# Optimization experiments

Measured on AMD Instinct MI355X. Metric: run time of the kernel, lower is better.

## Reference

```python
import jax, jax.numpy as jnp
from jax import lax
import numpy as np

B = 256
# conv stack: (in_ch, out_ch, kernel)
_CONV_CFG = [(1, 3, 4), (3, 9, 4), (9, 12, 4), (12, 15, 4), (15, 15, 3)]
_FLAT = 15 * 4 ** 4  # 3840, matches nn.Linear(15*(18-14)**4, 100)


def _conv4d(x, w, b):
    """True 4D valid convolution. x: [B,C,d1,d2,d3,d4], w: [O,I,k,k,k,k]."""
    dn = lax.conv_dimension_numbers(x.shape, w.shape, ('NCDHWX', 'OIDHWX', 'NCDHWX'))
    y = lax.conv_general_dilated(x, w, window_strides=(1, 1, 1, 1),
                                 padding='VALID', dimension_numbers=dn)
    return y + b.reshape((1, -1) + (1,) * 4)


def setup_inputs() -> dict:
    key = jax.random.key(0)
    ks = jax.random.split(key, 16)
    inp = {'x': jax.random.normal(ks[0], (B, 1, 18, 18, 18, 18), dtype=jnp.float32)}
    for i, (ci, co, k) in enumerate(_CONV_CFG, start=1):
        fan_in = ci * k ** 4
        inp[f'w{i}'] = jax.random.normal(ks[2 * i - 1], (co, ci, k, k, k, k), dtype=jnp.float32) / np.sqrt(fan_in)
        inp[f'b{i}'] = jnp.zeros((co,), dtype=jnp.float32)
    inp['fc1_w'] = jax.random.normal(ks[11], (_FLAT, 100), dtype=jnp.float32) / np.sqrt(_FLAT)
    inp['fc1_b'] = jnp.zeros((100,), dtype=jnp.float32)
    inp['fc2_w'] = jax.random.normal(ks[12], (100, 1), dtype=jnp.float32) / np.sqrt(100.0)
    inp['fc2_b'] = jnp.zeros((1,), dtype=jnp.float32)
    return inp


def reference(x, w1, b1, w2, b2, w3, b3, w4, b4, w5, b5, fc1_w, fc1_b, fc2_w, fc2_b):
    h = jax.nn.relu(_conv4d(x, w1, b1))
    h = jax.nn.relu(_conv4d(h, w2, b2))
    h = jax.nn.relu(_conv4d(h, w3, b3))
    h = jax.nn.relu(_conv4d(h, w4, b4))
    h = jax.nn.relu(_conv4d(h, w5, b5))  # [B,15,4,4,4,4]
    h = h.reshape(h.shape[0], -1)        # [B,3840], torch Flatten order
    # Dropout(0.5) is identity at inference (eval mode)
    h = jax.nn.relu(h @ fc1_w + fc1_b)
    return jax.nn.sigmoid(h @ fc2_w + fc2_b)  # [B,1]
```

## Files before the change

### kernel.cpp

```cpp
#include <hip/hip_runtime.h>
#include <hip/hip_bf16.h>


#define BATCH 256
typedef unsigned int u32;
typedef float    f32x4  __attribute__((ext_vector_type(4)));
typedef float    f32x16 __attribute__((ext_vector_type(16)));
typedef _Float16 f16x8  __attribute__((ext_vector_type(8)));

struct __attribute__((packed, aligned(4))) f16x8w { f16x8 v; };

__global__ void cvt_f32_f16(const float* __restrict__ in, _Float16* __restrict__ o, int n8) {
    int i = blockIdx.x * blockDim.x + threadIdx.x;
    if (i >= n8) return;
    const f32x4* p = (const f32x4*)(in + (size_t)i * 8);
    f32x4 a = p[0], b = p[1];
    f16x8 v;
    #pragma unroll
    for (int j = 0; j < 4; ++j) { v[j] = (_Float16)a[j]; v[4 + j] = (_Float16)b[j]; }
    *(f16x8*)(o + (size_t)i * 8) = v;
}

template<int COUT, int CIN, int KS, int S>
__global__ void prepack_v5(const float* __restrict__ w, _Float16* __restrict__ wf) {
    constexpr int STEPS = CIN * KS * 2 * KS;
    constexpr int TOT = STEPS * 512;
    int idx = blockIdx.x * 256 + threadIdx.x;
    if (idx >= TOT) return;
    int j    = idx & 7;
    int lane = (idx >> 3) & 63;
    int st   = idx >> 9;
    int k1 = st % KS;
    int r1 = st / KS;
    int k3p = r1 & 1;
    int r2  = r1 >> 1;
    int k2 = r2 % KS;
    int ci = r2 / KS;
    int gg = lane >> 5, col = lane & 31;
    int oc = col / S, s = col % S;
    int k3 = k3p * 2 + gg;
    int k4 = j - s;
    float v = 0.0f;
    if (oc < COUT && k3 < KS && k4 >= 0 && k4 < KS)
        v = w[((((oc * CIN + ci) * KS + k1) * KS + k2) * KS + k3) * KS + k4];
    wf[idx] = (_Float16)v;
}

template<int BYTES>
__device__ __forceinline__ void stage_b(const _Float16* gsrc, char* ldst, int tid) {
    constexpr int N16 = BYTES / 16;
    const int wv = tid >> 6, ln = tid & 63;
    #pragma unroll
    for (int it = 0; it * 256 < N16; ++it) {
        int u16 = it * 256 + (wv << 6);
        if (u16 < N16) {
            const char* gp = (const char*)gsrc + (size_t)(u16 + ln) * 16;
            __builtin_amdgcn_global_load_lds(
                (const __attribute__((address_space(1))) unsigned int*)gp,
                (__attribute__((address_space(3))) unsigned int*)(ldst + u16 * 16),
                16, 0, 0);
        }
    }
}

template<int CIN, int COUT, int KS, int DIN, int DP, int S, int OP, int T,
         int CG, int MINW>
__launch_bounds__(256, MINW)
__global__ void conv4d_v11(const _Float16* __restrict__ x,
                           const _Float16* __restrict__ wf,
                           const float* __restrict__ bias,
                           _Float16* __restrict__ out) {
    constexpr int DOUT = DIN - KS + 1;
    constexpr int NB   = (DOUT + S - 1) / S;
    constexpr int PCOL = DOUT * DOUT * NB;
    constexpr int NTC  = (PCOL + 31) / 32;
    constexpr int NG   = DOUT / T;
    static_assert(DOUT % T == 0, "T must divide DOUT");
    constexpr int XD2 = DIN * DP;
    constexpr int XD1 = DIN * XD2;
    constexpr int XCI = DIN * XD1;
    constexpr int GROUPS = CIN * KS * 2;
    static_assert(GROUPS % CG == 0, "CG must divide GROUPS");
    static_assert(CG % 2 == 0, "CG even so buffer parity gi&1 is consistent");
    constexpr int CSTEPS = CG * KS;
    constexpr int CBYTES = CSTEPS * 1024;
    constexpr int NCHUNK = GROUPS / CG;
    constexpr int NBUF   = (NCHUNK > 1) ? 2 : 1;
    constexpr int AJ = T + KS - 1;
    constexpr u32 NW   = (u32)BATCH * NG * NTC;
    constexpr u32 POUT = (u32)DOUT * DOUT * DOUT * OP;

    __shared__ char bsm[NBUF * CBYTES];
    const int tid = threadIdx.x;
    u32 wid = blockIdx.x * 4u + (u32)(tid >> 6);
    if (wid >= NW) wid = NW - 1u;
    const int ln = tid & 63;
    const int g  = ln >> 5;
    const int r  = ln & 31;

    u32 tc = wid % (u32)NTC;  u32 q = wid / (u32)NTC;
    u32 d1g = q % (u32)NG;    u32 b = q / (u32)NG;
    u32 rr = tc * 32u + (u32)r;  if (rr >= (u32)PCOL) rr = (u32)PCOL - 1u;
    u32 u  = rr % (u32)NB;    u32 q2 = rr / (u32)NB;
    u32 d3 = q2 % (u32)DOUT;  u32 d2 = q2 / (u32)DOUT;

    const u32 lanebase2 = (b * (u32)(CIN * XCI) + d1g * (u32)(T * XD1)
                         + d2 * (u32)XD2 + d3 * (u32)DP + (u32)(g * DP)
                         + u * (u32)S) * 2u;
    const char* xc = (const char*)x;

    f32x16 acc[T];
    #pragma unroll
    for (int t = 0; t < T; ++t)
        #pragma unroll
        for (int i = 0; i < 16; ++i) acc[t][i] = 0.0f;

    stage_b<CBYTES>(wf, &bsm[0], tid);

    f16x8 ar[2][AJ];
    {
        const char* ap0 = xc + lanebase2;
        #pragma unroll
        for (int j = 0; j < AJ; ++j)
            ar[0][j] = ((const f16x8w*)(ap0 + j * (XD1 * 2)))->v;
    }

    #pragma unroll 1
    for (int ch = 0; ch < NCHUNK; ++ch) {
        __syncthreads();
        if (NCHUNK > 1 && ch + 1 < NCHUNK)
            stage_b<CBYTES>(wf + (size_t)(ch + 1) * CSTEPS * 512,
                            &bsm[((ch + 1) & 1) * CBYTES], tid);
        const char* bb = &bsm[(ch & 1) * (NBUF > 1 ? CBYTES : 0)] + ln * 16;
        #pragma unroll
        for (int gi = 0; gi < CG; ++gi) {
            const int grp = ch * CG + gi;
            if (grp + 1 < GROUPS) {
                int g2  = grp + 1;
                int k3p = g2 & 1;
                int k2  = (g2 >> 1) % KS;
                int ci  = (g2 >> 1) / KS;
                u32 goff = ((u32)ci * (u32)XCI + (u32)k2 * (u32)XD2
                          + (u32)(k3p * 2 * DP)) * 2u;
                const char* ap = xc + lanebase2 + goff;
                #pragma unroll
                for (int j = 0; j < AJ; ++j)
                    ar[(gi + 1) & 1][j] = ((const f16x8w*)(ap + j * (XD1 * 2)))->v;
            }
            #pragma unroll
            for (int k1 = 0; k1 < KS; ++k1) {
                f16x8 bf = *(const f16x8*)(bb + (gi * KS + k1) * 1024);
                #pragma unroll
                for (int t = 0; t < T; ++t)
                    acc[t] = __builtin_amdgcn_mfma_f32_32x32x16_f16(
                        ar[gi & 1][k1 + t], bf, acc[t], 0, 0, 0);
            }
        }
    }

    const int oc = r / S, s = r % S;
    if (oc >= COUT) return;
    float bv = bias[oc];
    #pragma unroll
    for (int reg = 0; reg < 16; ++reg) {
        int rowoff = (reg & 3) + 8 * (reg >> 2) + 4 * g;
        u32 rr2 = tc * 32u + (u32)rowoff;
        if (rr2 >= (u32)PCOL) rr2 = (u32)PCOL - 1u;
        u32 uu = rr2 % (u32)NB;  u32 qq = rr2 / (u32)NB;
        u32 dd3 = qq % (u32)DOUT; u32 dd2 = qq / (u32)DOUT;
        u32 d4 = uu * (u32)S + (u32)s;
        if (d4 < (u32)DOUT) {
            u32 obase = (b * (u32)COUT + (u32)oc) * POUT
                      + (dd2 * (u32)DOUT + dd3) * (u32)OP + d4
                      + d1g * (u32)(T * DOUT * DOUT * OP);
            #pragma unroll
            for (int t = 0; t < T; ++t)
                out[obase + (u32)t * (u32)(DOUT * DOUT * OP)]
                    = (_Float16)fmaxf(acc[t][reg] + bv, 0.0f);
        }
    }
}

__global__ void prepack_fc1(const float* __restrict__ w, _Float16* __restrict__ wf) {
    int idx = blockIdx.x * 256 + threadIdx.x;
    if (idx >= 430080) return;
    int j    = idx & 7;
    int lane = (idx >> 3) & 63;
    int t9   = idx >> 9;
    int st   = t9 % 120;
    int ni   = t9 / 120;
    int k    = st * 32 + (lane >> 4) * 8 + j;
    int col  = ni * 16 + (lane & 15);
    wf[idx] = (_Float16)((col < 100) ? w[k * 100 + col] : 0.0f);
}

__launch_bounds__(256)
__global__ void fc1_mfma(const _Float16* __restrict__ h,
                         const _Float16* __restrict__ wfc,
                         const float* __restrict__ bias,
                         float* __restrict__ o) {
    int wv   = blockIdx.x * 4 + (threadIdx.x >> 6);
    int lane = threadIdx.x & 63;
    int r = lane & 15, g = lane >> 4;
    int mi = wv / 7, ni = wv % 7;
    const f16x8* A  = (const f16x8*)(h + (size_t)(mi * 16 + r) * 3840);
    const f16x8* Bv = (const f16x8*)wfc;
    f32x4 acc = {0.f, 0.f, 0.f, 0.f};
    #pragma unroll 4
    for (int st = 0; st < 120; ++st) {
        f16x8 a = A[st * 4 + g];
        f16x8 b = Bv[(ni * 120 + st) * 64 + lane];
        acc = __builtin_amdgcn_mfma_f32_16x16x32_f16(a, b, acc, 0, 0, 0);
    }
    int col = ni * 16 + r;
    if (col < 100) {
        float bv = bias[col];
        #pragma unroll
        for (int i = 0; i < 4; ++i) {
            int row = mi * 16 + g * 4 + i;
            o[row * 100 + col] = fmaxf(acc[i] + bv, 0.0f);
        }
    }
}

__global__ void fc2_sigmoid(const float* __restrict__ h,
                            const float* __restrict__ w,
                            const float* __restrict__ bias,
                            float* __restrict__ out) {
    int b = blockIdx.x * blockDim.x + threadIdx.x;
    if (b >= BATCH) return;
    const float* hb = h + b * 100;
    float acc = bias[0];
    #pragma unroll
    for (int j = 0; j < 100; ++j)
        acc = fmaf(hb[j], w[j], acc);
    out[b] = 1.0f / (1.0f + expf(-acc));
}

extern "C" void kernel_launch(void* const* d_in, const int* in_sizes, int n_in,
                              void* d_out, int out_size, void* d_ws, size_t ws_size,
                              hipStream_t stream) {
    const float* x    = (const float*)d_in[0];
    const float* w1   = (const float*)d_in[1];
    const float* b1   = (const float*)d_in[2];
    const float* w2   = (const float*)d_in[3];
    const float* b2   = (const float*)d_in[4];
    const float* w3   = (const float*)d_in[5];
    const float* b3   = (const float*)d_in[6];
    const float* w4   = (const float*)d_in[7];
    const float* b4   = (const float*)d_in[8];
    const float* w5   = (const float*)d_in[9];
    const float* b5   = (const float*)d_in[10];
    const float* fc1w = (const float*)d_in[11];
    const float* fc1b = (const float*)d_in[12];
    const float* fc2w = (const float*)d_in[13];
    const float* fc2b = (const float*)d_in[14];
    float* out = (float*)d_out;

    _Float16* W = (_Float16*)d_ws;
    size_t cur = 0;
    auto alloc = [&](size_t n) { _Float16* p = W + cur; cur += (n + 255) & ~(size_t)255; return p; };
    _Float16* x16 = alloc(26873856);
    _Float16* h1  = alloc(41472000);
    _Float16* h2  = alloc(47775744);
    _Float16* h3  = alloc(22394880);
    _Float16* h4  = alloc(4976640);
    _Float16* h5  = alloc(983040);
    _Float16* wf1 = alloc(16384);
    _Float16* wf2 = alloc(49152);
    _Float16* wf3 = alloc(147456);
    _Float16* wf4 = alloc(196608);
    _Float16* wf5 = alloc(138240);
    _Float16* wfc = alloc(430080);
    float* fc1out = (float*)alloc(51200 + 256);

    cvt_f32_f16<<<13122, 256, 0, stream>>>(x, x16, 3359232);

    prepack_v5<3, 1, 4, 4><<<64,  256, 0, stream>>>(w1, wf1);
    prepack_v5<9, 3, 4, 2><<<192, 256, 0, stream>>>(w2, wf2);
    prepack_v5<12, 9, 4, 2><<<576, 256, 0, stream>>>(w3, wf3);
    prepack_v5<15, 12, 4, 2><<<768, 256, 0, stream>>>(w4, wf4);
    prepack_v5<15, 15, 3, 2><<<540, 256, 0, stream>>>(w5, wf5);
    prepack_fc1<<<1680, 256, 0, stream>>>(fc1w, wfc);

    conv4d_v11<1, 3, 4, 18, 18, 4, 16, 3, 8, 3><<<9280, 256, 0, stream>>>(x16, wf1, b1, h1);
    conv4d_v11<3, 9, 4, 15, 16, 2, 12, 4, 4, 3><<<5184, 256, 0, stream>>>(h1, wf2, b2, h2);
    conv4d_v11<9, 12, 4, 12, 12, 2, 10, 3, 6, 3><<<2496, 256, 0, stream>>>(h2, wf3, b3, h3);
    conv4d_v11<12, 15, 4, 9, 10, 2, 6, 3, 6, 3><<<512, 256, 0, stream>>>(h3, wf4, b4, h4);
    conv4d_v11<15, 15, 3, 6, 6, 2, 4, 4, 6, 3><<<64, 256, 0, stream>>>(h4, wf5, b5, h5);

    fc1_mfma<<<28, 256, 0, stream>>>(h5, wfc, fc1b, fc1out);
    fc2_sigmoid<<<1, 256, 0, stream>>>(fc1out, fc2w, fc2b, out);
}
```

Measured before the change: 912.5 us.

## Load packed conv weights directly into registers instead of staging via LDS

The conv kernel no longer stages prepacked weight fragments into shared memory with global_load_lds and __syncthreads. Each lane now loads its B fragments straight from global memory (L1/L2-cached) into a double-buffered register array, prefetched one group ahead alongside the activation loads. This removes LDS usage and block-wide barriers, which may raise occupancy, at the cost of more VGPRs and redundant global traffic across waves. Layer 2 also changes its time tile from 4 to 3 with a matching larger grid.

```diff
diff --git a/kernel.cpp b/kernel.cpp
--- a/kernel.cpp
+++ b/kernel.cpp
@@ -46,27 +46,10 @@
     wf[idx] = (_Float16)v;
 }
 
-template<int BYTES>
-__device__ __forceinline__ void stage_b(const _Float16* gsrc, char* ldst, int tid) {
-    constexpr int N16 = BYTES / 16;
-    const int wv = tid >> 6, ln = tid & 63;
-    #pragma unroll
-    for (int it = 0; it * 256 < N16; ++it) {
-        int u16 = it * 256 + (wv << 6);
-        if (u16 < N16) {
-            const char* gp = (const char*)gsrc + (size_t)(u16 + ln) * 16;
-            __builtin_amdgcn_global_load_lds(
-                (const __attribute__((address_space(1))) unsigned int*)gp,
-                (__attribute__((address_space(3))) unsigned int*)(ldst + u16 * 16),
-                16, 0, 0);
-        }
-    }
-}
-
 template<int CIN, int COUT, int KS, int DIN, int DP, int S, int OP, int T,
-         int CG, int MINW>
+         int UB, int MINW>
 __launch_bounds__(256, MINW)
-__global__ void conv4d_v11(const _Float16* __restrict__ x,
+__global__ void conv4d_v12(const _Float16* __restrict__ x,
                            const _Float16* __restrict__ wf,
                            const float* __restrict__ bias,
                            _Float16* __restrict__ out) {
@@ -80,17 +63,13 @@
     constexpr int XD1 = DIN * XD2;
     constexpr int XCI = DIN * XD1;
     constexpr int GROUPS = CIN * KS * 2;
-    static_assert(GROUPS % CG == 0, "CG must divide GROUPS");
-    static_assert(CG % 2 == 0, "CG even so buffer parity gi&1 is consistent");
-    constexpr int CSTEPS = CG * KS;
-    constexpr int CBYTES = CSTEPS * 1024;
-    constexpr int NCHUNK = GROUPS / CG;
-    constexpr int NBUF   = (NCHUNK > 1) ? 2 : 1;
+    static_assert(GROUPS % UB == 0, "UB must divide GROUPS");
+    static_assert(UB % 2 == 0, "UB even so parity gi&1 is static");
+    constexpr int NOUTER = GROUPS / UB;
     constexpr int AJ = T + KS - 1;
     constexpr u32 NW   = (u32)BATCH * NG * NTC;
     constexpr u32 POUT = (u32)DOUT * DOUT * DOUT * OP;
 
-    __shared__ char bsm[NBUF * CBYTES];
     const int tid = threadIdx.x;
     u32 wid = blockIdx.x * 4u + (u32)(tid >> 6);
     if (wid >= NW) wid = NW - 1u;
@@ -108,6 +87,7 @@
                          + d2 * (u32)XD2 + d3 * (u32)DP + (u32)(g * DP)
                          + u * (u32)S) * 2u;
     const char* xc = (const char*)x;
+    const f16x8* wfv = (const f16x8*)wf;
 
     f32x16 acc[T];
     #pragma unroll
@@ -115,26 +95,26 @@
         #pragma unroll
         for (int i = 0; i < 16; ++i) acc[t][i] = 0.0f;
 
-    stage_b<CBYTES>(wf, &bsm[0], tid);
-
     f16x8 ar[2][AJ];
+    f16x8 bfb[2][KS];
     {
         const char* ap0 = xc + lanebase2;
         #pragma unroll
         for (int j = 0; j < AJ; ++j)
             ar[0][j] = ((const f16x8w*)(ap0 + j * (XD1 * 2)))->v;
+        #pragma unroll
+        for (int k1 = 0; k1 < KS; ++k1)
+            bfb[0][k1] = wfv[k1 * 64 + ln];
     }
 
     #pragma unroll 1
-    for (int ch = 0; ch < NCHUNK; ++ch) {
-        __syncthreads();
-        if (NCHUNK > 1 && ch + 1 < NCHUNK)
-            stage_b<CBYTES>(wf + (size_t)(ch + 1) * CSTEPS * 512,
-                            &bsm[((ch + 1) & 1) * CBYTES], tid);
-        const char* bb = &bsm[(ch & 1) * (NBUF > 1 ? CBYTES : 0)] + ln * 16;
-        #pragma unroll
-        for (int gi = 0; gi < CG; ++gi) {
-            const int grp = ch * CG + gi;
+    for (int c = 0; c < NOUTER; ++c) {
+        #pragma unroll
+        for (int gi = 0; gi < UB; ++gi) {
+            const int grp = c * UB + gi;
+            constexpr int P0 = 0;  (void)P0;
+            const int pcur = gi & 1;
+            const int pnxt = (gi + 1) & 1;
             if (grp + 1 < GROUPS) {
                 int g2  = grp + 1;
                 int k3p = g2 & 1;
@@ -145,15 +125,17 @@
                 const char* ap = xc + lanebase2 + goff;
                 #pragma unroll
                 for (int j = 0; j < AJ; ++j)
-                    ar[(gi + 1) & 1][j] = ((const f16x8w*)(ap + j * (XD1 * 2)))->v;
+                    ar[pnxt][j] = ((const f16x8w*)(ap + j * (XD1 * 2)))->v;
+                #pragma unroll
+                for (int k1 = 0; k1 < KS; ++k1)
+                    bfb[pnxt][k1] = wfv[(size_t)(g2 * KS + k1) * 64 + ln];
             }
             #pragma unroll
             for (int k1 = 0; k1 < KS; ++k1) {
-                f16x8 bf = *(const f16x8*)(bb + (gi * KS + k1) * 1024);
                 #pragma unroll
                 for (int t = 0; t < T; ++t)
                     acc[t] = __builtin_amdgcn_mfma_f32_32x32x16_f16(
-                        ar[gi & 1][k1 + t], bf, acc[t], 0, 0, 0);
+                        ar[pcur][k1 + t], bfb[pcur][k1], acc[t], 0, 0, 0);
             }
         }
     }
@@ -283,11 +265,11 @@
     prepack_v5<15, 15, 3, 2><<<540, 256, 0, stream>>>(w5, wf5);
     prepack_fc1<<<1680, 256, 0, stream>>>(fc1w, wfc);
 
-    conv4d_v11<1, 3, 4, 18, 18, 4, 16, 3, 8, 3><<<9280, 256, 0, stream>>>(x16, wf1, b1, h1);
-    conv4d_v11<3, 9, 4, 15, 16, 2, 12, 4, 4, 3><<<5184, 256, 0, stream>>>(h1, wf2, b2, h2);
-    conv4d_v11<9, 12, 4, 12, 12, 2, 10, 3, 6, 3><<<2496, 256, 0, stream>>>(h2, wf3, b3, h3);
-    conv4d_v11<12, 15, 4, 9, 10, 2, 6, 3, 6, 3><<<512, 256, 0, stream>>>(h3, wf4, b4, h4);
-    conv4d_v11<15, 15, 3, 6, 6, 2, 4, 4, 6, 3><<<64, 256, 0, stream>>>(h4, wf5, b5, h5);
+    conv4d_v12<1, 3, 4, 18, 18, 4, 16, 3, 8, 3><<<9280, 256, 0, stream>>>(x16, wf1, b1, h1);
+    conv4d_v12<3, 9, 4, 15, 16, 2, 12, 3, 6, 3><<<6912, 256, 0, stream>>>(h1, wf2, b2, h2);
+    conv4d_v12<9, 12, 4, 12, 12, 2, 10, 3, 6, 3><<<2496, 256, 0, stream>>>(h2, wf3, b3, h3);
+    conv4d_v12<12, 15, 4, 9, 10, 2, 6, 3, 6, 3><<<512, 256, 0, stream>>>(h3, wf4, b4, h4);
+    conv4d_v12<15, 15, 3, 6, 6, 2, 4, 4, 6, 3><<<64, 256, 0, stream>>>(h4, wf5, b5, h5);
 
     fc1_mfma<<<28, 256, 0, stream>>>(h5, wfc, fc1b, fc1out);
     fc2_sigmoid<<<1, 256, 0, stream>>>(fc1out, fc2w, fc2b, out);
```

Result: slower. 1.027 ms (+12.6%).
